# Kernel optimization log

Measured on AMD Instinct MI355X. Metric: run time of the kernel, lower is better.

The kernel has to match this reference:

```python
import jax, jax.numpy as jnp
from jax import lax
import numpy as np

VOCAB, EMB, HID, NCLS = 50257, 768, 512, 5
B, T = 32, 1024


def setup_inputs() -> dict:
    key = jax.random.key(0)
    ks = jax.random.split(key, 12)
    s_e = 1.0  # torch nn.Embedding default init is N(0,1)
    def unif(k, shape, fan):
        bound = 1.0 / np.sqrt(fan)
        return jax.random.uniform(k, shape, jnp.float32, -bound, bound)
    return {
        "x": jax.random.randint(ks[0], (B, T), 0, VOCAB),
        "emb": jax.random.normal(ks[1], (VOCAB, EMB), jnp.float32) * s_e,
        "w_ih0": unif(ks[2], (4 * HID, EMB), HID),
        "w_hh0": unif(ks[3], (4 * HID, HID), HID),
        "b_ih0": unif(ks[4], (4 * HID,), HID),
        "b_hh0": unif(ks[5], (4 * HID,), HID),
        "w_ih1": unif(ks[6], (4 * HID, HID), HID),
        "w_hh1": unif(ks[7], (4 * HID, HID), HID),
        "b_ih1": unif(ks[8], (4 * HID,), HID),
        "b_hh1": unif(ks[9], (4 * HID,), HID),
        "fc_w": unif(ks[10], (NCLS, HID), HID),
        "fc_b": unif(ks[11], (NCLS,), HID),
    }


def _lstm_layer(x, w_ih, w_hh, b_ih, b_hh):
    # x: [B, T, D] -> hs: [B, T, H]; PyTorch gate order: i, f, g, o
    Bb = x.shape[0]
    H = w_hh.shape[1]
    gx = jnp.einsum('btd,gd->btg', x, w_ih) + b_ih + b_hh  # [B, T, 4H]
    gx_t = jnp.swapaxes(gx, 0, 1)  # [T, B, 4H]
    h0 = jnp.zeros((Bb, H), x.dtype)
    c0 = jnp.zeros((Bb, H), x.dtype)

    def step(carry, g_in):
        h, c = carry
        g = g_in + h @ w_hh.T
        i, f, gg, o = jnp.split(g, 4, axis=-1)
        c = jax.nn.sigmoid(f) * c + jax.nn.sigmoid(i) * jnp.tanh(gg)
        h = jax.nn.sigmoid(o) * jnp.tanh(c)
        return (h, c), h

    _, hs = lax.scan(step, (h0, c0), gx_t)
    return jnp.swapaxes(hs, 0, 1)  # [B, T, H]


def reference(x, emb, w_ih0, w_hh0, b_ih0, b_hh0, w_ih1, w_hh1, b_ih1, b_hh1, fc_w, fc_b):
    e = emb[x]                                   # [B, T, EMB]
    h1 = _lstm_layer(e, w_ih0, w_hh0, b_ih0, b_hh0)   # [B, T, H]
    # inter-layer dropout and final dropout are identity in eval mode
    h2 = _lstm_layer(h1, w_ih1, w_hh1, b_ih1, b_hh1)  # [B, T, H]
    last = h2[:, -1, :]                          # [B, H]
    return last @ fc_w.T + fc_b                  # [B, NCLS]
```

## Files before the change

### kernel.cpp

```cpp
#include <hip/hip_runtime.h>
#include <stdint.h>

typedef _Float16 f16;
typedef _Float16 half8 __attribute__((ext_vector_type(8)));
typedef float f32x4 __attribute__((ext_vector_type(4)));
typedef unsigned long long u64;

#define T_SEQ 1024
#define NWG 136
#define FS 32

#define WS_FLAGS_BYTES (NWG * 128)
#define WS_H0 32768
#define WS_H1 (WS_H0 + 131072)
#define WS_E  (WS_H1 + 65536)
#define ESLOT 24576
#define HPLANE 16384

static __device__ __forceinline__ half8 ld_h8(const f16* p) {
    u64 lo = __hip_atomic_load((const u64*)p,     __ATOMIC_RELAXED, __HIP_MEMORY_SCOPE_AGENT);
    u64 hi = __hip_atomic_load((const u64*)p + 1, __ATOMIC_RELAXED, __HIP_MEMORY_SCOPE_AGENT);
    union { u64 q[2]; half8 v; } u; u.q[0] = lo; u.q[1] = hi; return u.v;
}

static __device__ __forceinline__ void poll64(uint32_t* flags, int base, int n,
                                              uint32_t need, int lane) {
    int idx = (base + (lane < n ? lane : 0)) * FS;
    while (true) {
        uint32_t v = __hip_atomic_load(flags + idx, __ATOMIC_RELAXED,
                                       __HIP_MEMORY_SCOPE_AGENT);
        if (__all(v >= need)) break;
        __builtin_amdgcn_s_sleep(1);
    }
    __builtin_amdgcn_sched_barrier(0);
}

static __device__ __forceinline__ void poll2(uint32_t* flags, uint32_t needA,
                                             uint32_t needB, int lane) {
    while (true) {
        uint32_t a = __hip_atomic_load(flags + lane * FS, __ATOMIC_RELAXED,
                                       __HIP_MEMORY_SCOPE_AGENT);
        uint32_t b = __hip_atomic_load(flags + (64 + lane) * FS, __ATOMIC_RELAXED,
                                       __HIP_MEMORY_SCOPE_AGENT);
        if (__all((a >= needA) && (b >= needB))) break;
        __builtin_amdgcn_s_sleep(1);
    }
    __builtin_amdgcn_sched_barrier(0);
}

__global__ void __launch_bounds__(256, 1)
lstm_fused(const int* __restrict__ x, const float* __restrict__ emb,
           const float* __restrict__ w_ih0, const float* __restrict__ w_hh0,
           const float* __restrict__ b_ih0, const float* __restrict__ b_hh0,
           const float* __restrict__ w_ih1, const float* __restrict__ w_hh1,
           const float* __restrict__ b_ih1, const float* __restrict__ b_hh1,
           const float* __restrict__ fc_w, const float* __restrict__ fc_b,
           float* __restrict__ out, uint8_t* __restrict__ ws)
{
    const int wg   = blockIdx.x;
    const int tid  = threadIdx.x;
    const int lane = tid & 63;
    const int wave = tid >> 6;
    const int mtile = wave >> 1;
    const int ntile = wave & 1;
    const int r8   = lane & 15;
    const int kgb  = lane >> 4;

    uint32_t* flags = (uint32_t*)ws;
    f16* h0buf = (f16*)(ws + WS_H0);
    f16* h1buf = (f16*)(ws + WS_H1);
    f16* ering = (f16*)(ws + WS_E);

    if (wg >= 128) {
        const int p = wg - 128;
        auto gather = [&](int t) {
#pragma unroll
            for (int rr = 0; rr < 2; ++rr) {
                int idx = rr * 256 + tid;
                if (idx < 384) {
                    int bl = idx / 96, seg = idx % 96, k0 = seg * 8;
                    int b = p * 4 + bl;
                    int tok = x[b * T_SEQ + t];
                    const float* src = emb + (size_t)tok * 768 + k0;
                    float4 v0 = ((const float4*)src)[0];
                    float4 v1 = ((const float4*)src)[1];
                    union { half8 h; u64 q[2]; } u;
                    u.h[0] = (f16)v0.x; u.h[1] = (f16)v0.y; u.h[2] = (f16)v0.z; u.h[3] = (f16)v0.w;
                    u.h[4] = (f16)v1.x; u.h[5] = (f16)v1.y; u.h[6] = (f16)v1.z; u.h[7] = (f16)v1.w;
                    u64* dst = (u64*)(ering + (size_t)(t & 3) * ESLOT + ((size_t)seg * 32 + b) * 8);
                    __hip_atomic_store(dst,     u.q[0], __ATOMIC_RELAXED, __HIP_MEMORY_SCOPE_AGENT);
                    __hip_atomic_store(dst + 1, u.q[1], __ATOMIC_RELAXED, __HIP_MEMORY_SCOPE_AGENT);
                }
            }
        };
        gather(0); gather(1); gather(2);
        asm volatile("s_waitcnt vmcnt(0)" ::: "memory");
        __syncthreads();
        if (tid == 0)
            __hip_atomic_store(flags + wg * FS, 3u, __ATOMIC_RELAXED, __HIP_MEMORY_SCOPE_AGENT);
        for (int s = 0;; ++s) {
            int g = s + 3;
            if (g >= T_SEQ) {
                if (tid == 0)
                    __hip_atomic_store(flags + wg * FS, (uint32_t)(T_SEQ + 8),
                                       __ATOMIC_RELAXED, __HIP_MEMORY_SCOPE_AGENT);
                break;
            }
            poll64(flags, 0, 64, (uint32_t)(s + 1), lane);
            gather(g);
            asm volatile("s_waitcnt vmcnt(0)" ::: "memory");
            __syncthreads();
            if (tid == 0)
                __hip_atomic_store(flags + wg * FS, (uint32_t)(s + 4),
                                   __ATOMIC_RELAXED, __HIP_MEMORY_SCOPE_AGENT);
        }
        return;
    }

    const bool isL0 = (wg < 64);
    const int wloc  = isL0 ? wg : wg - 64;
    const int j0    = wloc * 8;

    __shared__ float accs[32][33];
    __shared__ float bias_lds[32];
    __shared__ f16   hsh[32][8];
    __shared__ f16   stage[16384];

    const int nrow = ((ntile * 2 + (r8 >> 3)) << 9) + j0 + (r8 & 7);
    half8 breg[40];
    if (isL0) {
#pragma unroll
        for (int kc = 0; kc < 40; ++kc) {
            int k = kc * 32 + kgb * 8;
            const float* src = (k < 768) ? (w_ih0 + (size_t)nrow * 768 + k)
                                         : (w_hh0 + (size_t)nrow * 512 + (k - 768));
            half8 v;
#pragma unroll
            for (int e = 0; e < 8; ++e) v[e] = (f16)src[e];
            breg[kc] = v;
        }
    } else {
#pragma unroll
        for (int kc = 0; kc < 32; ++kc) {
            int k = kc * 32 + kgb * 8;
            const float* src = (k < 512) ? (w_ih1 + (size_t)nrow * 512 + k)
                                         : (w_hh1 + (size_t)nrow * 512 + (k - 512));
            half8 v;
#pragma unroll
            for (int e = 0; e < 8; ++e) v[e] = (f16)src[e];
            breg[kc] = v;
        }
    }
    if (tid < 32) {
        int n2 = ((tid >> 3) << 9) + j0 + (tid & 7);
        bias_lds[tid] = isL0 ? (b_ih0[n2] + b_hh0[n2]) : (b_ih1[n2] + b_hh1[n2]);
    }

    {
        int gid = wg * 256 + tid;
        if (gid < 8192) {
            u64* base = (gid < 4096) ? (u64*)(h0buf + 3 * HPLANE)
                                     : (u64*)(h1buf + 1 * HPLANE);
            __hip_atomic_store(base + (gid & 4095), 0ULL,
                               __ATOMIC_RELAXED, __HIP_MEMORY_SCOPE_AGENT);
        }
    }
    asm volatile("s_waitcnt vmcnt(0)" ::: "memory");
    __syncthreads();
    if (tid == 0)
        __hip_atomic_store(flags + wg * FS, isL0 ? 1u : 2u,
                           __ATOMIC_RELAXED, __HIP_MEMORY_SCOPE_AGENT);

    float cst = 0.f;
    const int tb = tid >> 3, tj = tid & 7;
    const int arow = mtile * 16 + r8;

    const int sBeg = isL0 ? 0 : 1;
    const int sEnd = isL0 ? T_SEQ : T_SEQ + 1;

    for (int s = sBeg; s < sEnd; ++s) {
        f32x4 acc0 = {0.f, 0.f, 0.f, 0.f}, acc1 = {0.f, 0.f, 0.f, 0.f};
        if (isL0) {
            poll64(flags, 128, 8, (uint32_t)(s + 1), lane);
            const f16* pe = ering + (size_t)(s & 3) * ESLOT;
            half8 ea[24];
#pragma unroll
            for (int kc = 0; kc < 24; ++kc)
                ea[kc] = ld_h8(pe + (((size_t)(kc * 4 + kgb) * 32 + arow) << 3));
            poll2(flags, (uint32_t)(s + 1), (uint32_t)(s > 0 ? s - 1 : 0), lane);
            const f16* ph = h0buf + (size_t)((s + 3) & 3) * HPLANE;
#pragma unroll
            for (int kc = 0; kc < 24; ++kc) {
                if (kc & 1) acc1 = __builtin_amdgcn_mfma_f32_16x16x32_f16(ea[kc], breg[kc], acc1, 0, 0, 0);
                else        acc0 = __builtin_amdgcn_mfma_f32_16x16x32_f16(ea[kc], breg[kc], acc0, 0, 0, 0);
            }
#pragma unroll
            for (int kc = 24; kc < 40; ++kc) {
                half8 a = ld_h8(ph + ((((size_t)(kc - 24) * 4 + kgb) * 32 + arow) << 3));
                if (kc & 1) acc1 = __builtin_amdgcn_mfma_f32_16x16x32_f16(a, breg[kc], acc1, 0, 0, 0);
                else        acc0 = __builtin_amdgcn_mfma_f32_16x16x32_f16(a, breg[kc], acc0, 0, 0, 0);
            }
        } else {
            poll64(flags, 0, 64, (uint32_t)(s + 1), lane);
            const f16* pa = h0buf + (size_t)((s + 3) & 3) * HPLANE;
            half8 av[16];
#pragma unroll
            for (int kc = 0; kc < 16; ++kc)
                av[kc] = ld_h8(pa + (((size_t)(kc * 4 + kgb) * 32 + arow) << 3));
            poll64(flags, 64, 64, (uint32_t)(s + 1), lane);
            const f16* pb = h1buf + (size_t)(s & 1) * HPLANE;
#pragma unroll
            for (int kc = 0; kc < 16; ++kc) {
                if (kc & 1) acc1 = __builtin_amdgcn_mfma_f32_16x16x32_f16(av[kc], breg[kc], acc1, 0, 0, 0);
                else        acc0 = __builtin_amdgcn_mfma_f32_16x16x32_f16(av[kc], breg[kc], acc0, 0, 0, 0);
            }
#pragma unroll
            for (int kc = 16; kc < 32; ++kc) {
                half8 a = ld_h8(pb + ((((size_t)(kc - 16) * 4 + kgb) * 32 + arow) << 3));
                if (kc & 1) acc1 = __builtin_amdgcn_mfma_f32_16x16x32_f16(a, breg[kc], acc1, 0, 0, 0);
                else        acc0 = __builtin_amdgcn_mfma_f32_16x16x32_f16(a, breg[kc], acc0, 0, 0, 0);
            }
        }
        {
            f32x4 accv = acc0 + acc1;
            const int crow0 = mtile * 16 + (lane >> 4) * 4;
            const int ccol  = ntile * 16 + r8;
#pragma unroll
            for (int q = 0; q < 4; ++q) accs[crow0 + q][ccol] = accv[q];
        }
        __syncthreads();
        {
            float gi = accs[tb][tj]      + bias_lds[tj];
            float gf = accs[tb][8 + tj]  + bias_lds[8 + tj];
            float gg = accs[tb][16 + tj] + bias_lds[16 + tj];
            float go = accs[tb][24 + tj] + bias_lds[24 + tj];
            float si = __builtin_amdgcn_rcpf(1.f + __expf(-gi));
            float sf = __builtin_amdgcn_rcpf(1.f + __expf(-gf));
            float so = __builtin_amdgcn_rcpf(1.f + __expf(-go));
            float tg = 1.f - 2.f * __builtin_amdgcn_rcpf(__expf(2.f * gg) + 1.f);
            cst = sf * cst + si * tg;
            float hv = so * (1.f - 2.f * __builtin_amdgcn_rcpf(__expf(2.f * cst) + 1.f));
            hsh[tb][tj] = (f16)hv;
        }
        __syncthreads();
        if (tid < 32) {
            f16* plane = isL0 ? (h0buf + (size_t)(s & 3) * HPLANE)
                              : (h1buf + (size_t)((s + 1) & 1) * HPLANE);
            u64* dst = (u64*)plane + ((size_t)wloc * 32 + tid) * 2;
            const u64* srcp = (const u64*)hsh + tid * 2;
            u64 q0 = srcp[0], q1 = srcp[1];
            __hip_atomic_store(dst,     q0, __ATOMIC_RELAXED, __HIP_MEMORY_SCOPE_AGENT);
            __hip_atomic_store(dst + 1, q1, __ATOMIC_RELAXED, __HIP_MEMORY_SCOPE_AGENT);
        }
        if (tid == 0) {
            asm volatile("s_waitcnt vmcnt(0)" ::: "memory");
            __hip_atomic_store(flags + wg * FS, (uint32_t)(s + 2),
                               __ATOMIC_RELAXED, __HIP_MEMORY_SCOPE_AGENT);
        }
    }

    if (wg == 0) {
        poll64(flags, 64, 64, (uint32_t)(T_SEQ + 2), lane);
        u64* h2g = (u64*)(h1buf + 1 * HPLANE);
        u64* stg = (u64*)stage;
        for (int i = tid; i < 4096; i += 256)
            stg[i] = __hip_atomic_load(h2g + i, __ATOMIC_RELAXED, __HIP_MEMORY_SCOPE_AGENT);
        __syncthreads();
        if (tid < 160) {
            int b = tid / 5, n = tid % 5;
            const f16* h2 = stage;
            float fsum = fc_b[n];
#pragma unroll 8
            for (int j = 0; j < 512; ++j)
                fsum += (float)h2[((j >> 3) * 32 + b) * 8 + (j & 7)] * fc_w[n * 512 + j];
            out[b * 5 + n] = fsum;
        }
    }
}

extern "C" void kernel_launch(void* const* d_in, const int* in_sizes, int n_in,
                              void* d_out, int out_size, void* d_ws, size_t ws_size,
                              hipStream_t stream) {
    (void)in_sizes; (void)n_in; (void)out_size; (void)ws_size;
    hipMemsetAsync(d_ws, 0, WS_FLAGS_BYTES, stream);
    lstm_fused<<<dim3(NWG), dim3(256), 0, stream>>>(
        (const int*)d_in[0],  (const float*)d_in[1],
        (const float*)d_in[2], (const float*)d_in[3],
        (const float*)d_in[4], (const float*)d_in[5],
        (const float*)d_in[6], (const float*)d_in[7],
        (const float*)d_in[8], (const float*)d_in[9],
        (const float*)d_in[10], (const float*)d_in[11],
        (float*)d_out, (uint8_t*)d_ws);
}
```

Baseline: 4.309 ms.

## Stage LSTM weights in LDS, poll flags with one wave, pack flag slots

Recurrent and input weights now live in 80KB of shared memory instead of 160 VGPRs per lane. They are loaded once by two waves and read from LDS at every MFMA step. Flag polling is done by wave 0 only, followed by a workgroup barrier. The flag stride shrinks from 32 to 8 words, so polls touch fewer cache lines. All A-operand loads for the hidden state are issued before the MFMA chains to hide load latency. In exchange, every timestep pays for LDS weight reads and extra barriers on a recurrence that is bound by latency.

```diff
diff --git a/kernel.cpp b/kernel.cpp
--- a/kernel.cpp
+++ b/kernel.cpp
@@ -8,9 +8,9 @@
 
 #define T_SEQ 1024
 #define NWG 136
-#define FS 32
-
-#define WS_FLAGS_BYTES (NWG * 128)
+#define FS 8
+
+#define WS_FLAGS_BYTES 8192
 #define WS_H0 32768
 #define WS_H1 (WS_H0 + 131072)
 #define WS_E  (WS_H1 + 65536)
@@ -106,7 +106,8 @@
                                        __ATOMIC_RELAXED, __HIP_MEMORY_SCOPE_AGENT);
                 break;
             }
-            poll64(flags, 0, 64, (uint32_t)(s + 1), lane);
+            if (wave == 0) poll64(flags, 0, 64, (uint32_t)(s + 1), lane);
+            __syncthreads();
             gather(g);
             asm volatile("s_waitcnt vmcnt(0)" ::: "memory");
             __syncthreads();
@@ -121,34 +122,35 @@
     const int wloc  = isL0 ? wg : wg - 64;
     const int j0    = wloc * 8;
 
+    __shared__ half8 wlds[2 * 40 * 64];
     __shared__ float accs[32][33];
     __shared__ float bias_lds[32];
     __shared__ f16   hsh[32][8];
-    __shared__ f16   stage[16384];
 
     const int nrow = ((ntile * 2 + (r8 >> 3)) << 9) + j0 + (r8 & 7);
-    half8 breg[40];
-    if (isL0) {
-#pragma unroll
-        for (int kc = 0; kc < 40; ++kc) {
-            int k = kc * 32 + kgb * 8;
-            const float* src = (k < 768) ? (w_ih0 + (size_t)nrow * 768 + k)
-                                         : (w_hh0 + (size_t)nrow * 512 + (k - 768));
-            half8 v;
-#pragma unroll
-            for (int e = 0; e < 8; ++e) v[e] = (f16)src[e];
-            breg[kc] = v;
-        }
-    } else {
-#pragma unroll
-        for (int kc = 0; kc < 32; ++kc) {
-            int k = kc * 32 + kgb * 8;
-            const float* src = (k < 512) ? (w_ih1 + (size_t)nrow * 512 + k)
-                                         : (w_hh1 + (size_t)nrow * 512 + (k - 512));
-            half8 v;
-#pragma unroll
-            for (int e = 0; e < 8; ++e) v[e] = (f16)src[e];
-            breg[kc] = v;
+    if (wave < 2) {
+        if (isL0) {
+#pragma unroll
+            for (int kc = 0; kc < 40; ++kc) {
+                int k = kc * 32 + kgb * 8;
+                const float* src = (k < 768) ? (w_ih0 + (size_t)nrow * 768 + k)
+                                             : (w_hh0 + (size_t)nrow * 512 + (k - 768));
+                half8 v;
+#pragma unroll
+                for (int e = 0; e < 8; ++e) v[e] = (f16)src[e];
+                wlds[ntile * 2560 + kc * 64 + lane] = v;
+            }
+        } else {
+#pragma unroll
+            for (int kc = 0; kc < 32; ++kc) {
+                int k = kc * 32 + kgb * 8;
+                const float* src = (k < 512) ? (w_ih1 + (size_t)nrow * 512 + k)
+                                             : (w_hh1 + (size_t)nrow * 512 + (k - 512));
+                half8 v;
+#pragma unroll
+                for (int e = 0; e < 8; ++e) v[e] = (f16)src[e];
+                wlds[ntile * 2560 + kc * 64 + lane] = v;
+            }
         }
     }
     if (tid < 32) {
@@ -174,6 +176,7 @@
     float cst = 0.f;
     const int tb = tid >> 3, tj = tid & 7;
     const int arow = mtile * 16 + r8;
+    const half8* wbase = wlds + ntile * 2560;
 
     const int sBeg = isL0 ? 0 : 1;
     const int sEnd = isL0 ? T_SEQ : T_SEQ + 1;
@@ -181,44 +184,58 @@
     for (int s = sBeg; s < sEnd; ++s) {
         f32x4 acc0 = {0.f, 0.f, 0.f, 0.f}, acc1 = {0.f, 0.f, 0.f, 0.f};
         if (isL0) {
-            poll64(flags, 128, 8, (uint32_t)(s + 1), lane);
+            if (wave == 0) poll64(flags, 128, 8, (uint32_t)(s + 1), lane);
+            __syncthreads();
             const f16* pe = ering + (size_t)(s & 3) * ESLOT;
             half8 ea[24];
 #pragma unroll
             for (int kc = 0; kc < 24; ++kc)
                 ea[kc] = ld_h8(pe + (((size_t)(kc * 4 + kgb) * 32 + arow) << 3));
-            poll2(flags, (uint32_t)(s + 1), (uint32_t)(s > 0 ? s - 1 : 0), lane);
+            if (wave == 0) poll2(flags, (uint32_t)(s + 1), (uint32_t)(s > 0 ? s - 1 : 0), lane);
+            __syncthreads();
             const f16* ph = h0buf + (size_t)((s + 3) & 3) * HPLANE;
+            half8 av[16];
+#pragma unroll
+            for (int kc = 0; kc < 16; ++kc)
+                av[kc] = ld_h8(ph + (((size_t)(kc * 4 + kgb) * 32 + arow) << 3));
 #pragma unroll
             for (int kc = 0; kc < 24; ++kc) {
-                if (kc & 1) acc1 = __builtin_amdgcn_mfma_f32_16x16x32_f16(ea[kc], breg[kc], acc1, 0, 0, 0);
-                else        acc0 = __builtin_amdgcn_mfma_f32_16x16x32_f16(ea[kc], breg[kc], acc0, 0, 0, 0);
-            }
-#pragma unroll
-            for (int kc = 24; kc < 40; ++kc) {
-                half8 a = ld_h8(ph + ((((size_t)(kc - 24) * 4 + kgb) * 32 + arow) << 3));
-                if (kc & 1) acc1 = __builtin_amdgcn_mfma_f32_16x16x32_f16(a, breg[kc], acc1, 0, 0, 0);
-                else        acc0 = __builtin_amdgcn_mfma_f32_16x16x32_f16(a, breg[kc], acc0, 0, 0, 0);
+                half8 bw = wbase[kc * 64 + lane];
+                if (kc & 1) acc1 = __builtin_amdgcn_mfma_f32_16x16x32_f16(ea[kc], bw, acc1, 0, 0, 0);
+                else        acc0 = __builtin_amdgcn_mfma_f32_16x16x32_f16(ea[kc], bw, acc0, 0, 0, 0);
+            }
+#pragma unroll
+            for (int kc = 0; kc < 16; ++kc) {
+                half8 bw = wbase[(24 + kc) * 64 + lane];
+                if (kc & 1) acc1 = __builtin_amdgcn_mfma_f32_16x16x32_f16(av[kc], bw, acc1, 0, 0, 0);
+                else        acc0 = __builtin_amdgcn_mfma_f32_16x16x32_f16(av[kc], bw, acc0, 0, 0, 0);
             }
         } else {
-            poll64(flags, 0, 64, (uint32_t)(s + 1), lane);
+            if (wave == 0) poll64(flags, 0, 64, (uint32_t)(s + 1), lane);
+            __syncthreads();
             const f16* pa = h0buf + (size_t)((s + 3) & 3) * HPLANE;
             half8 av[16];
 #pragma unroll
             for (int kc = 0; kc < 16; ++kc)
                 av[kc] = ld_h8(pa + (((size_t)(kc * 4 + kgb) * 32 + arow) << 3));
-            poll64(flags, 64, 64, (uint32_t)(s + 1), lane);
+            if (wave == 0) poll64(flags, 64, 64, (uint32_t)(s + 1), lane);
+            __syncthreads();
             const f16* pb = h1buf + (size_t)(s & 1) * HPLANE;
+            half8 bv[16];
+#pragma unroll
+            for (int kc = 0; kc < 16; ++kc)
+                bv[kc] = ld_h8(pb + (((size_t)(kc * 4 + kgb) * 32 + arow) << 3));
 #pragma unroll
             for (int kc = 0; kc < 16; ++kc) {
-                if (kc & 1) acc1 = __builtin_amdgcn_mfma_f32_16x16x32_f16(av[kc], breg[kc], acc1, 0, 0, 0);
-                else        acc0 = __builtin_amdgcn_mfma_f32_16x16x32_f16(av[kc], breg[kc], acc0, 0, 0, 0);
-            }
-#pragma unroll
-            for (int kc = 16; kc < 32; ++kc) {
-                half8 a = ld_h8(pb + ((((size_t)(kc - 16) * 4 + kgb) * 32 + arow) << 3));
-                if (kc & 1) acc1 = __builtin_amdgcn_mfma_f32_16x16x32_f16(a, breg[kc], acc1, 0, 0, 0);
-                else        acc0 = __builtin_amdgcn_mfma_f32_16x16x32_f16(a, breg[kc], acc0, 0, 0, 0);
+                half8 bw = wbase[kc * 64 + lane];
+                if (kc & 1) acc1 = __builtin_amdgcn_mfma_f32_16x16x32_f16(av[kc], bw, acc1, 0, 0, 0);
+                else        acc0 = __builtin_amdgcn_mfma_f32_16x16x32_f16(av[kc], bw, acc0, 0, 0, 0);
+            }
+#pragma unroll
+            for (int kc = 0; kc < 16; ++kc) {
+                half8 bw = wbase[(16 + kc) * 64 + lane];
+                if (kc & 1) acc1 = __builtin_amdgcn_mfma_f32_16x16x32_f16(bv[kc], bw, acc1, 0, 0, 0);
+                else        acc0 = __builtin_amdgcn_mfma_f32_16x16x32_f16(bv[kc], bw, acc0, 0, 0, 0);
             }
         }
         {
@@ -260,15 +277,16 @@
     }
 
     if (wg == 0) {
-        poll64(flags, 64, 64, (uint32_t)(T_SEQ + 2), lane);
+        if (wave == 0) poll64(flags, 64, 64, (uint32_t)(T_SEQ + 2), lane);
+        __syncthreads();
         u64* h2g = (u64*)(h1buf + 1 * HPLANE);
-        u64* stg = (u64*)stage;
+        u64* stg = (u64*)wlds;
         for (int i = tid; i < 4096; i += 256)
             stg[i] = __hip_atomic_load(h2g + i, __ATOMIC_RELAXED, __HIP_MEMORY_SCOPE_AGENT);
         __syncthreads();
         if (tid < 160) {
             int b = tid / 5, n = tid % 5;
-            const f16* h2 = stage;
+            const f16* h2 = (const f16*)stg;
             float fsum = fc_b[n];
 #pragma unroll 8
             for (int j = 0; j < 512; ++j)
```

Result: slower. 4.781 ms (+10.9%).

## Replace per-workgroup flag polling with slotted atomic counters and deeper h1 ring

Applied to the files above, without the earlier changes.

Replaces the per-workgroup flag array, which consumers polled across 64 lanes, with per-timestep slot counters: 8 counters per ring slot, each incremented by a group of 8 producer workgroups, so a wait reads only 16 words. The h1 buffer becomes a 4-deep ring, which loosens the coupling between layers, and L0 now loads its h operands up front before the MFMAs. Embedding producers signal through per-slot counters. The intent is less polling traffic and latency on the per-step critical path. In exchange it adds atomic fetch_add contention and relies on counter wraparound across 8 slots being correct, and several vmcnt waits were dropped before signaling, which risks memory-ordering bugs.

```diff
diff --git a/kernel.cpp b/kernel.cpp
--- a/kernel.cpp
+++ b/kernel.cpp
@@ -8,14 +8,18 @@
 
 #define T_SEQ 1024
 #define NWG 136
-#define FS 32
-
-#define WS_FLAGS_BYTES (NWG * 128)
-#define WS_H0 32768
+
+#define R0L(slot) ((uint32_t*)(ws + ((((slot) & 7)) * 128)))
+#define R1L(slot) ((uint32_t*)(ws + 1024 + ((((slot) & 7)) * 128)))
+#define WS_H0 4096
 #define WS_H1 (WS_H0 + 131072)
-#define WS_E  (WS_H1 + 65536)
+#define WS_E  (WS_H1 + 131072)
 #define ESLOT 24576
 #define HPLANE 16384
+
+static __device__ __forceinline__ uint32_t needOf(int it) {
+    return it < 0 ? 0u : 8u * (((uint32_t)it >> 3) + 1u);
+}
 
 static __device__ __forceinline__ half8 ld_h8(const f16* p) {
     u64 lo = __hip_atomic_load((const u64*)p,     __ATOMIC_RELAXED, __HIP_MEMORY_SCOPE_AGENT);
@@ -23,26 +27,21 @@
     union { u64 q[2]; half8 v; } u; u.q[0] = lo; u.q[1] = hi; return u.v;
 }
 
-static __device__ __forceinline__ void poll64(uint32_t* flags, int base, int n,
-                                              uint32_t need, int lane) {
-    int idx = (base + (lane < n ? lane : 0)) * FS;
+static __device__ __forceinline__ void poll1(uint32_t* w, uint32_t need) {
+    while (__hip_atomic_load(w, __ATOMIC_RELAXED, __HIP_MEMORY_SCOPE_AGENT) < need)
+        __builtin_amdgcn_s_sleep(1);
+    __builtin_amdgcn_sched_barrier(0);
+}
+
+static __device__ __forceinline__ void poll16(uint32_t* a, uint32_t na,
+                                              uint32_t* b, uint32_t nb, int lane) {
+    uint32_t* addr; uint32_t need;
+    if (lane < 8)       { addr = a + lane;       need = na; }
+    else if (lane < 16) { addr = b + (lane - 8); need = nb; }
+    else                { addr = a;              need = 0;  }
     while (true) {
-        uint32_t v = __hip_atomic_load(flags + idx, __ATOMIC_RELAXED,
-                                       __HIP_MEMORY_SCOPE_AGENT);
+        uint32_t v = __hip_atomic_load(addr, __ATOMIC_RELAXED, __HIP_MEMORY_SCOPE_AGENT);
         if (__all(v >= need)) break;
-        __builtin_amdgcn_s_sleep(1);
-    }
-    __builtin_amdgcn_sched_barrier(0);
-}
-
-static __device__ __forceinline__ void poll2(uint32_t* flags, uint32_t needA,
-                                             uint32_t needB, int lane) {
-    while (true) {
-        uint32_t a = __hip_atomic_load(flags + lane * FS, __ATOMIC_RELAXED,
-                                       __HIP_MEMORY_SCOPE_AGENT);
-        uint32_t b = __hip_atomic_load(flags + (64 + lane) * FS, __ATOMIC_RELAXED,
-                                       __HIP_MEMORY_SCOPE_AGENT);
-        if (__all((a >= needA) && (b >= needB))) break;
         __builtin_amdgcn_s_sleep(1);
     }
     __builtin_amdgcn_sched_barrier(0);
@@ -66,7 +65,8 @@
     const int r8   = lane & 15;
     const int kgb  = lane >> 4;
 
-    uint32_t* flags = (uint32_t*)ws;
+    uint32_t* EW = (uint32_t*)(ws + 2048);
+    uint32_t* IW = (uint32_t*)(ws + 2176);
     f16* h0buf = (f16*)(ws + WS_H0);
     f16* h1buf = (f16*)(ws + WS_H1);
     f16* ering = (f16*)(ws + WS_E);
@@ -94,25 +94,20 @@
             }
         };
         gather(0); gather(1); gather(2);
-        asm volatile("s_waitcnt vmcnt(0)" ::: "memory");
         __syncthreads();
-        if (tid == 0)
-            __hip_atomic_store(flags + wg * FS, 3u, __ATOMIC_RELAXED, __HIP_MEMORY_SCOPE_AGENT);
-        for (int s = 0;; ++s) {
-            int g = s + 3;
-            if (g >= T_SEQ) {
-                if (tid == 0)
-                    __hip_atomic_store(flags + wg * FS, (uint32_t)(T_SEQ + 8),
-                                       __ATOMIC_RELAXED, __HIP_MEMORY_SCOPE_AGENT);
-                break;
-            }
-            poll64(flags, 0, 64, (uint32_t)(s + 1), lane);
+        if (tid == 0) {
+            __hip_atomic_fetch_add(EW + 0, 1u, __ATOMIC_RELAXED, __HIP_MEMORY_SCOPE_AGENT);
+            __hip_atomic_fetch_add(EW + 1, 1u, __ATOMIC_RELAXED, __HIP_MEMORY_SCOPE_AGENT);
+            __hip_atomic_fetch_add(EW + 2, 1u, __ATOMIC_RELAXED, __HIP_MEMORY_SCOPE_AGENT);
+        }
+        for (int g = 3; g < T_SEQ; ++g) {
+            if (g >= 4)
+                poll16(R0L(g - 4), needOf(g - 4), R0L(g - 4), 0u, lane);
             gather(g);
-            asm volatile("s_waitcnt vmcnt(0)" ::: "memory");
             __syncthreads();
             if (tid == 0)
-                __hip_atomic_store(flags + wg * FS, (uint32_t)(s + 4),
-                                   __ATOMIC_RELAXED, __HIP_MEMORY_SCOPE_AGENT);
+                __hip_atomic_fetch_add(EW + (g & 3), 1u,
+                                       __ATOMIC_RELAXED, __HIP_MEMORY_SCOPE_AGENT);
         }
         return;
     }
@@ -160,108 +155,113 @@
         int gid = wg * 256 + tid;
         if (gid < 8192) {
             u64* base = (gid < 4096) ? (u64*)(h0buf + 3 * HPLANE)
-                                     : (u64*)(h1buf + 1 * HPLANE);
+                                     : (u64*)(h1buf + 3 * HPLANE);
             __hip_atomic_store(base + (gid & 4095), 0ULL,
                                __ATOMIC_RELAXED, __HIP_MEMORY_SCOPE_AGENT);
         }
     }
-    asm volatile("s_waitcnt vmcnt(0)" ::: "memory");
     __syncthreads();
-    if (tid == 0)
-        __hip_atomic_store(flags + wg * FS, isL0 ? 1u : 2u,
-                           __ATOMIC_RELAXED, __HIP_MEMORY_SCOPE_AGENT);
+    if (wg < 32 && tid == 0)
+        __hip_atomic_fetch_add(IW, 1u, __ATOMIC_RELAXED, __HIP_MEMORY_SCOPE_AGENT);
+    poll1(IW, 32u);
 
     float cst = 0.f;
     const int tb = tid >> 3, tj = tid & 7;
     const int arow = mtile * 16 + r8;
 
-    const int sBeg = isL0 ? 0 : 1;
     const int sEnd = isL0 ? T_SEQ : T_SEQ + 1;
 
-    for (int s = sBeg; s < sEnd; ++s) {
-        f32x4 acc0 = {0.f, 0.f, 0.f, 0.f}, acc1 = {0.f, 0.f, 0.f, 0.f};
-        if (isL0) {
-            poll64(flags, 128, 8, (uint32_t)(s + 1), lane);
-            const f16* pe = ering + (size_t)(s & 3) * ESLOT;
-            half8 ea[24];
-#pragma unroll
-            for (int kc = 0; kc < 24; ++kc)
-                ea[kc] = ld_h8(pe + (((size_t)(kc * 4 + kgb) * 32 + arow) << 3));
-            poll2(flags, (uint32_t)(s + 1), (uint32_t)(s > 0 ? s - 1 : 0), lane);
-            const f16* ph = h0buf + (size_t)((s + 3) & 3) * HPLANE;
-#pragma unroll
-            for (int kc = 0; kc < 24; ++kc) {
-                if (kc & 1) acc1 = __builtin_amdgcn_mfma_f32_16x16x32_f16(ea[kc], breg[kc], acc1, 0, 0, 0);
-                else        acc0 = __builtin_amdgcn_mfma_f32_16x16x32_f16(ea[kc], breg[kc], acc0, 0, 0, 0);
-            }
-#pragma unroll
-            for (int kc = 24; kc < 40; ++kc) {
-                half8 a = ld_h8(ph + ((((size_t)(kc - 24) * 4 + kgb) * 32 + arow) << 3));
-                if (kc & 1) acc1 = __builtin_amdgcn_mfma_f32_16x16x32_f16(a, breg[kc], acc1, 0, 0, 0);
-                else        acc0 = __builtin_amdgcn_mfma_f32_16x16x32_f16(a, breg[kc], acc0, 0, 0, 0);
-            }
-        } else {
-            poll64(flags, 0, 64, (uint32_t)(s + 1), lane);
-            const f16* pa = h0buf + (size_t)((s + 3) & 3) * HPLANE;
-            half8 av[16];
-#pragma unroll
-            for (int kc = 0; kc < 16; ++kc)
-                av[kc] = ld_h8(pa + (((size_t)(kc * 4 + kgb) * 32 + arow) << 3));
-            poll64(flags, 64, 64, (uint32_t)(s + 1), lane);
-            const f16* pb = h1buf + (size_t)(s & 1) * HPLANE;
-#pragma unroll
-            for (int kc = 0; kc < 16; ++kc) {
-                if (kc & 1) acc1 = __builtin_amdgcn_mfma_f32_16x16x32_f16(av[kc], breg[kc], acc1, 0, 0, 0);
-                else        acc0 = __builtin_amdgcn_mfma_f32_16x16x32_f16(av[kc], breg[kc], acc0, 0, 0, 0);
-            }
-#pragma unroll
-            for (int kc = 16; kc < 32; ++kc) {
-                half8 a = ld_h8(pb + ((((size_t)(kc - 16) * 4 + kgb) * 32 + arow) << 3));
-                if (kc & 1) acc1 = __builtin_amdgcn_mfma_f32_16x16x32_f16(a, breg[kc], acc1, 0, 0, 0);
-                else        acc0 = __builtin_amdgcn_mfma_f32_16x16x32_f16(a, breg[kc], acc0, 0, 0, 0);
-            }
-        }
-        {
-            f32x4 accv = acc0 + acc1;
-            const int crow0 = mtile * 16 + (lane >> 4) * 4;
-            const int ccol  = ntile * 16 + r8;
-#pragma unroll
-            for (int q = 0; q < 4; ++q) accs[crow0 + q][ccol] = accv[q];
-        }
-        __syncthreads();
-        {
-            float gi = accs[tb][tj]      + bias_lds[tj];
-            float gf = accs[tb][8 + tj]  + bias_lds[8 + tj];
-            float gg = accs[tb][16 + tj] + bias_lds[16 + tj];
-            float go = accs[tb][24 + tj] + bias_lds[24 + tj];
-            float si = __builtin_amdgcn_rcpf(1.f + __expf(-gi));
-            float sf = __builtin_amdgcn_rcpf(1.f + __expf(-gf));
-            float so = __builtin_amdgcn_rcpf(1.f + __expf(-go));
-            float tg = 1.f - 2.f * __builtin_amdgcn_rcpf(__expf(2.f * gg) + 1.f);
-            cst = sf * cst + si * tg;
-            float hv = so * (1.f - 2.f * __builtin_amdgcn_rcpf(__expf(2.f * cst) + 1.f));
-            hsh[tb][tj] = (f16)hv;
-        }
-        __syncthreads();
-        if (tid < 32) {
-            f16* plane = isL0 ? (h0buf + (size_t)(s & 3) * HPLANE)
-                              : (h1buf + (size_t)((s + 1) & 1) * HPLANE);
-            u64* dst = (u64*)plane + ((size_t)wloc * 32 + tid) * 2;
-            const u64* srcp = (const u64*)hsh + tid * 2;
-            u64 q0 = srcp[0], q1 = srcp[1];
-            __hip_atomic_store(dst,     q0, __ATOMIC_RELAXED, __HIP_MEMORY_SCOPE_AGENT);
-            __hip_atomic_store(dst + 1, q1, __ATOMIC_RELAXED, __HIP_MEMORY_SCOPE_AGENT);
+    for (int s = 0; s < sEnd; ++s) {
+        const bool active = isL0 || (s >= 1);
+        if (active) {
+            f32x4 acc0 = {0.f, 0.f, 0.f, 0.f}, acc1 = {0.f, 0.f, 0.f, 0.f};
+            if (isL0) {
+                poll1(EW + (s & 3), 8u * (((uint32_t)s >> 2) + 1u));
+                const f16* pe = ering + (size_t)(s & 3) * ESLOT;
+                half8 ea[24];
+#pragma unroll
+                for (int kc = 0; kc < 24; ++kc)
+                    ea[kc] = ld_h8(pe + (((size_t)(kc * 4 + kgb) * 32 + arow) << 3));
+                poll16(R0L(s - 1), needOf(s - 1), R1L(s - 3), needOf(s - 3), lane);
+                const f16* ph = h0buf + (size_t)((s + 3) & 3) * HPLANE;
+                half8 av[16];
+#pragma unroll
+                for (int kc = 0; kc < 16; ++kc)
+                    av[kc] = ld_h8(ph + (((size_t)(kc * 4 + kgb) * 32 + arow) << 3));
+#pragma unroll
+                for (int kc = 0; kc < 24; ++kc) {
+                    if (kc & 1) acc1 = __builtin_amdgcn_mfma_f32_16x16x32_f16(ea[kc], breg[kc], acc1, 0, 0, 0);
+                    else        acc0 = __builtin_amdgcn_mfma_f32_16x16x32_f16(ea[kc], breg[kc], acc0, 0, 0, 0);
+                }
+#pragma unroll
+                for (int kc = 0; kc < 16; ++kc) {
+                    if (kc & 1) acc1 = __builtin_amdgcn_mfma_f32_16x16x32_f16(av[kc], breg[24 + kc], acc1, 0, 0, 0);
+                    else        acc0 = __builtin_amdgcn_mfma_f32_16x16x32_f16(av[kc], breg[24 + kc], acc0, 0, 0, 0);
+                }
+            } else {
+                poll16(R0L(s - 1), needOf(s - 1), R1L(s - 1), needOf(s - 1), lane);
+                const f16* pa = h0buf + (size_t)((s + 3) & 3) * HPLANE;
+                const f16* pb = h1buf + (size_t)((s + 2) & 3) * HPLANE;
+                half8 av[16], bv[16];
+#pragma unroll
+                for (int kc = 0; kc < 16; ++kc)
+                    av[kc] = ld_h8(pa + (((size_t)(kc * 4 + kgb) * 32 + arow) << 3));
+#pragma unroll
+                for (int kc = 0; kc < 16; ++kc)
+                    bv[kc] = ld_h8(pb + (((size_t)(kc * 4 + kgb) * 32 + arow) << 3));
+#pragma unroll
+                for (int kc = 0; kc < 16; ++kc) {
+                    if (kc & 1) acc1 = __builtin_amdgcn_mfma_f32_16x16x32_f16(av[kc], breg[kc], acc1, 0, 0, 0);
+                    else        acc0 = __builtin_amdgcn_mfma_f32_16x16x32_f16(av[kc], breg[kc], acc0, 0, 0, 0);
+                }
+#pragma unroll
+                for (int kc = 0; kc < 16; ++kc) {
+                    if (kc & 1) acc1 = __builtin_amdgcn_mfma_f32_16x16x32_f16(bv[kc], breg[16 + kc], acc1, 0, 0, 0);
+                    else        acc0 = __builtin_amdgcn_mfma_f32_16x16x32_f16(bv[kc], breg[16 + kc], acc0, 0, 0, 0);
+                }
+            }
+            {
+                f32x4 accv = acc0 + acc1;
+                const int crow0 = mtile * 16 + (lane >> 4) * 4;
+                const int ccol  = ntile * 16 + r8;
+#pragma unroll
+                for (int q = 0; q < 4; ++q) accs[crow0 + q][ccol] = accv[q];
+            }
+            __syncthreads();
+            {
+                float gi = accs[tb][tj]      + bias_lds[tj];
+                float gf = accs[tb][8 + tj]  + bias_lds[8 + tj];
+                float gg = accs[tb][16 + tj] + bias_lds[16 + tj];
+                float go = accs[tb][24 + tj] + bias_lds[24 + tj];
+                float si = __builtin_amdgcn_rcpf(1.f + __expf(-gi));
+                float sf = __builtin_amdgcn_rcpf(1.f + __expf(-gf));
+                float so = __builtin_amdgcn_rcpf(1.f + __expf(-go));
+                float tg = 1.f - 2.f * __builtin_amdgcn_rcpf(__expf(2.f * gg) + 1.f);
+                cst = sf * cst + si * tg;
+                float hv = so * (1.f - 2.f * __builtin_amdgcn_rcpf(__expf(2.f * cst) + 1.f));
+                hsh[tb][tj] = (f16)hv;
+            }
+            __syncthreads();
+            if (tid < 32) {
+                f16* plane = isL0 ? (h0buf + (size_t)(s & 3) * HPLANE)
+                                  : (h1buf + (size_t)((s + 3) & 3) * HPLANE);
+                u64* dst = (u64*)plane + ((size_t)wloc * 32 + tid) * 2;
+                const u64* srcp = (const u64*)hsh + tid * 2;
+                u64 q0 = srcp[0], q1 = srcp[1];
+                __hip_atomic_store(dst,     q0, __ATOMIC_RELAXED, __HIP_MEMORY_SCOPE_AGENT);
+                __hip_atomic_store(dst + 1, q1, __ATOMIC_RELAXED, __HIP_MEMORY_SCOPE_AGENT);
+            }
         }
         if (tid == 0) {
             asm volatile("s_waitcnt vmcnt(0)" ::: "memory");
-            __hip_atomic_store(flags + wg * FS, (uint32_t)(s + 2),
-                               __ATOMIC_RELAXED, __HIP_MEMORY_SCOPE_AGENT);
+            uint32_t* ctr = (isL0 ? R0L(s) : R1L(s)) + (wloc >> 3);
+            __hip_atomic_fetch_add(ctr, 1u, __ATOMIC_RELAXED, __HIP_MEMORY_SCOPE_AGENT);
         }
     }
 
     if (wg == 0) {
-        poll64(flags, 64, 64, (uint32_t)(T_SEQ + 2), lane);
-        u64* h2g = (u64*)(h1buf + 1 * HPLANE);
+        poll16(R1L(0), needOf(T_SEQ), R1L(0), needOf(T_SEQ), lane);
+        u64* h2g = (u64*)(h1buf + 3 * HPLANE);
         u64* stg = (u64*)stage;
         for (int i = tid; i < 4096; i += 256)
             stg[i] = __hip_atomic_load(h2g + i, __ATOMIC_RELAXED, __HIP_MEMORY_SCOPE_AGENT);
@@ -282,7 +282,7 @@
                               void* d_out, int out_size, void* d_ws, size_t ws_size,
                               hipStream_t stream) {
     (void)in_sizes; (void)n_in; (void)out_size; (void)ws_size;
-    hipMemsetAsync(d_ws, 0, WS_FLAGS_BYTES, stream);
+    hipMemsetAsync(d_ws, 0, 4096, stream);
     lstm_fused<<<dim3(NWG), dim3(256), 0, stream>>>(
         (const int*)d_in[0],  (const float*)d_in[1],
         (const float*)d_in[2], (const float*)d_in[3],
```

Result: slower. 5.227 ms (+21.3%).

## Split flag arrays, use single combined poll, and stage A operands cooperatively in LDS

Applied to the files above, without the earlier changes.

Flags move into separate compact arrays for layer-0, layer-1 and the producer workgroups, packed at 32-byte stride instead of 128. Each step now waits on all dependencies in one combined poll. Every wave then loads a disjoint slice of the shared A operand (embeddings and hidden states) from global memory into LDS, so waves sharing an M tile no longer load the same data twice. The embedding ring shrinks to 3 slots and the producers key off layer-0 progress directly. This cuts redundant global loads per step, but adds an LDS round trip and a barrier, and removes the overlap between embedding loads and the hidden-state wait.

```diff
diff --git a/kernel.cpp b/kernel.cpp
--- a/kernel.cpp
+++ b/kernel.cpp
@@ -8,41 +8,60 @@
 
 #define T_SEQ 1024
 #define NWG 136
-#define FS 32
-
-#define WS_FLAGS_BYTES (NWG * 128)
-#define WS_H0 32768
+#define FS 8
+#define DE 3
+#define HPLANE 16384
+#define ESLOT 24576
+
+#define OFF_FA 0
+#define OFF_FB 2048
+#define OFF_FP 4096
+#define WS_H0 8192
 #define WS_H1 (WS_H0 + 131072)
 #define WS_E  (WS_H1 + 65536)
-#define ESLOT 24576
-#define HPLANE 16384
-
+
+static __device__ __forceinline__ u64 ld64(const u64* p) {
+    return __hip_atomic_load(p, __ATOMIC_RELAXED, __HIP_MEMORY_SCOPE_AGENT);
+}
+static __device__ __forceinline__ void st64(u64* p, u64 v) {
+    __hip_atomic_store(p, v, __ATOMIC_RELAXED, __HIP_MEMORY_SCOPE_AGENT);
+}
+static __device__ __forceinline__ uint32_t ld32(const uint32_t* p) {
+    return __hip_atomic_load(p, __ATOMIC_RELAXED, __HIP_MEMORY_SCOPE_AGENT);
+}
+static __device__ __forceinline__ void st32(uint32_t* p, uint32_t v) {
+    __hip_atomic_store(p, v, __ATOMIC_RELAXED, __HIP_MEMORY_SCOPE_AGENT);
+}
+static __device__ __forceinline__ half8 h8(u64 lo, u64 hi) {
+    union { u64 q[2]; half8 v; } u; u.q[0] = lo; u.q[1] = hi; return u.v;
+}
 static __device__ __forceinline__ half8 ld_h8(const f16* p) {
-    u64 lo = __hip_atomic_load((const u64*)p,     __ATOMIC_RELAXED, __HIP_MEMORY_SCOPE_AGENT);
-    u64 hi = __hip_atomic_load((const u64*)p + 1, __ATOMIC_RELAXED, __HIP_MEMORY_SCOPE_AGENT);
-    union { u64 q[2]; half8 v; } u; u.q[0] = lo; u.q[1] = hi; return u.v;
-}
-
-static __device__ __forceinline__ void poll64(uint32_t* flags, int base, int n,
-                                              uint32_t need, int lane) {
-    int idx = (base + (lane < n ? lane : 0)) * FS;
+    u64 lo = ld64((const u64*)p);
+    u64 hi = ld64((const u64*)p + 1);
+    return h8(lo, hi);
+}
+static __device__ __forceinline__ void pollM(const uint32_t* fA, uint32_t needA,
+                                             const uint32_t* fB, uint32_t needB,
+                                             const uint32_t* fP, uint32_t needP,
+                                             int lane) {
+    const uint32_t* pa = fA + (size_t)lane * FS;
+    const uint32_t* pb = fB + (size_t)lane * FS;
+    const uint32_t* pp = fP + (size_t)(lane & 7) * FS;
     while (true) {
-        uint32_t v = __hip_atomic_load(flags + idx, __ATOMIC_RELAXED,
-                                       __HIP_MEMORY_SCOPE_AGENT);
+        uint32_t va = ld32(pa);
+        uint32_t vb = ld32(pb);
+        uint32_t vp = ld32(pp);
+        if (__all((va >= needA) && (vb >= needB) && (vp >= needP))) break;
+        __builtin_amdgcn_s_sleep(1);
+    }
+    __builtin_amdgcn_sched_barrier(0);
+}
+static __device__ __forceinline__ void pollA(const uint32_t* flags, int n,
+                                             uint32_t need, int lane) {
+    const uint32_t* p = flags + (size_t)(lane < n ? lane : 0) * FS;
+    while (true) {
+        uint32_t v = ld32(p);
         if (__all(v >= need)) break;
-        __builtin_amdgcn_s_sleep(1);
-    }
-    __builtin_amdgcn_sched_barrier(0);
-}
-
-static __device__ __forceinline__ void poll2(uint32_t* flags, uint32_t needA,
-                                             uint32_t needB, int lane) {
-    while (true) {
-        uint32_t a = __hip_atomic_load(flags + lane * FS, __ATOMIC_RELAXED,
-                                       __HIP_MEMORY_SCOPE_AGENT);
-        uint32_t b = __hip_atomic_load(flags + (64 + lane) * FS, __ATOMIC_RELAXED,
-                                       __HIP_MEMORY_SCOPE_AGENT);
-        if (__all((a >= needA) && (b >= needB))) break;
         __builtin_amdgcn_s_sleep(1);
     }
     __builtin_amdgcn_sched_barrier(0);
@@ -65,20 +84,23 @@
     const int ntile = wave & 1;
     const int r8   = lane & 15;
     const int kgb  = lane >> 4;
-
-    uint32_t* flags = (uint32_t*)ws;
+    const int tb = tid >> 3, tj = tid & 7;
+
+    uint32_t* fA = (uint32_t*)(ws + OFF_FA);
+    uint32_t* fB = (uint32_t*)(ws + OFF_FB);
+    uint32_t* fP = (uint32_t*)(ws + OFF_FP);
     f16* h0buf = (f16*)(ws + WS_H0);
     f16* h1buf = (f16*)(ws + WS_H1);
     f16* ering = (f16*)(ws + WS_E);
 
     if (wg >= 128) {
         const int p = wg - 128;
-        auto gather = [&](int t) {
+        auto gather = [&](int t, int slot) {
 #pragma unroll
             for (int rr = 0; rr < 2; ++rr) {
-                int idx = rr * 256 + tid;
-                if (idx < 384) {
-                    int bl = idx / 96, seg = idx % 96, k0 = seg * 8;
+                int idx2 = rr * 256 + tid;
+                if (idx2 < 384) {
+                    int bl = idx2 / 96, seg = idx2 % 96, k0 = seg * 8;
                     int b = p * 4 + bl;
                     int tok = x[b * T_SEQ + t];
                     const float* src = emb + (size_t)tok * 768 + k0;
@@ -87,32 +109,21 @@
                     union { half8 h; u64 q[2]; } u;
                     u.h[0] = (f16)v0.x; u.h[1] = (f16)v0.y; u.h[2] = (f16)v0.z; u.h[3] = (f16)v0.w;
                     u.h[4] = (f16)v1.x; u.h[5] = (f16)v1.y; u.h[6] = (f16)v1.z; u.h[7] = (f16)v1.w;
-                    u64* dst = (u64*)(ering + (size_t)(t & 3) * ESLOT + ((size_t)seg * 32 + b) * 8);
-                    __hip_atomic_store(dst,     u.q[0], __ATOMIC_RELAXED, __HIP_MEMORY_SCOPE_AGENT);
-                    __hip_atomic_store(dst + 1, u.q[1], __ATOMIC_RELAXED, __HIP_MEMORY_SCOPE_AGENT);
+                    u64* dst = (u64*)(ering + (size_t)slot * ESLOT + ((size_t)seg * 32 + b) * 8);
+                    st64(dst, u.q[0]); st64(dst + 1, u.q[1]);
                 }
             }
         };
-        gather(0); gather(1); gather(2);
+        gather(0, 0); gather(1, 1); gather(2, 2);
         asm volatile("s_waitcnt vmcnt(0)" ::: "memory");
         __syncthreads();
-        if (tid == 0)
-            __hip_atomic_store(flags + wg * FS, 3u, __ATOMIC_RELAXED, __HIP_MEMORY_SCOPE_AGENT);
-        for (int s = 0;; ++s) {
-            int g = s + 3;
-            if (g >= T_SEQ) {
-                if (tid == 0)
-                    __hip_atomic_store(flags + wg * FS, (uint32_t)(T_SEQ + 8),
-                                       __ATOMIC_RELAXED, __HIP_MEMORY_SCOPE_AGENT);
-                break;
-            }
-            poll64(flags, 0, 64, (uint32_t)(s + 1), lane);
-            gather(g);
+        if (tid == 0) st32(fP + p * FS, 3u);
+        for (int g = 3; g < T_SEQ; ++g) {
+            pollA(fA, 64, (uint32_t)(g - 1), lane);
+            gather(g, g % DE);
             asm volatile("s_waitcnt vmcnt(0)" ::: "memory");
             __syncthreads();
-            if (tid == 0)
-                __hip_atomic_store(flags + wg * FS, (uint32_t)(s + 4),
-                                   __ATOMIC_RELAXED, __HIP_MEMORY_SCOPE_AGENT);
+            if (tid == 0) st32(fP + p * FS, (uint32_t)(g + 1));
         }
         return;
     }
@@ -121,10 +132,10 @@
     const int wloc  = isL0 ? wg : wg - 64;
     const int j0    = wloc * 8;
 
+    __shared__ half8 astage[80 * 64];
     __shared__ float accs[32][33];
     __shared__ float bias_lds[32];
     __shared__ f16   hsh[32][8];
-    __shared__ f16   stage[16384];
 
     const int nrow = ((ntile * 2 + (r8 >> 3)) << 9) + j0 + (r8 & 7);
     half8 breg[40];
@@ -161,70 +172,59 @@
         if (gid < 8192) {
             u64* base = (gid < 4096) ? (u64*)(h0buf + 3 * HPLANE)
                                      : (u64*)(h1buf + 1 * HPLANE);
-            __hip_atomic_store(base + (gid & 4095), 0ULL,
-                               __ATOMIC_RELAXED, __HIP_MEMORY_SCOPE_AGENT);
+            st64(base + (gid & 4095), 0ULL);
         }
     }
     asm volatile("s_waitcnt vmcnt(0)" ::: "memory");
     __syncthreads();
-    if (tid == 0)
-        __hip_atomic_store(flags + wg * FS, isL0 ? 1u : 2u,
-                           __ATOMIC_RELAXED, __HIP_MEMORY_SCOPE_AGENT);
+    if (tid == 0) st32((isL0 ? fA : fB) + wloc * FS, isL0 ? 1u : 2u);
 
     float cst = 0.f;
-    const int tb = tid >> 3, tj = tid & 7;
-    const int arow = mtile * 16 + r8;
+    const int crow0 = mtile * 16 + (lane >> 4) * 4;
+    const int ccol  = ntile * 16 + r8;
 
     const int sBeg = isL0 ? 0 : 1;
     const int sEnd = isL0 ? T_SEQ : T_SEQ + 1;
+    const int NKC  = isL0 ? 40 : 32;
+    const int NST  = isL0 ? 20 : 16;
 
     for (int s = sBeg; s < sEnd; ++s) {
+        if (isL0) pollM(fA, (uint32_t)(s + 1), fB, (uint32_t)(s > 0 ? s - 1 : 0),
+                        fP, (uint32_t)(s + 1), lane);
+        else      pollM(fA, (uint32_t)(s + 1), fB, (uint32_t)(s + 1),
+                        fP, 0u, lane);
+        const f16* pe = ering + (size_t)(s % DE) * ESLOT;
+        const f16* ph0 = h0buf + (size_t)((s + 3) & 3) * HPLANE;
+        const f16* ph1 = h1buf + (size_t)(s & 1) * HPLANE;
+        {
+            half8 stg[20];
+#pragma unroll
+            for (int j = 0; j < 20; ++j) {
+                if (j >= NST) break;
+                int f = wave * NST + j;
+                int mt = f / NKC, kc = f % NKC;
+                const f16* base; int kk;
+                if (isL0) { base = (kc < 24) ? pe : ph0; kk = (kc < 24) ? kc : kc - 24; }
+                else      { base = (kc < 16) ? ph0 : ph1; kk = (kc < 16) ? kc : kc - 16; }
+                stg[j] = ld_h8(base + (((size_t)(kk * 4 + kgb) * 32 + mt * 16 + r8) << 3));
+            }
+#pragma unroll
+            for (int j = 0; j < 20; ++j) {
+                if (j >= NST) break;
+                astage[(size_t)(wave * NST + j) * 64 + lane] = stg[j];
+            }
+        }
+        __syncthreads();
         f32x4 acc0 = {0.f, 0.f, 0.f, 0.f}, acc1 = {0.f, 0.f, 0.f, 0.f};
-        if (isL0) {
-            poll64(flags, 128, 8, (uint32_t)(s + 1), lane);
-            const f16* pe = ering + (size_t)(s & 3) * ESLOT;
-            half8 ea[24];
-#pragma unroll
-            for (int kc = 0; kc < 24; ++kc)
-                ea[kc] = ld_h8(pe + (((size_t)(kc * 4 + kgb) * 32 + arow) << 3));
-            poll2(flags, (uint32_t)(s + 1), (uint32_t)(s > 0 ? s - 1 : 0), lane);
-            const f16* ph = h0buf + (size_t)((s + 3) & 3) * HPLANE;
-#pragma unroll
-            for (int kc = 0; kc < 24; ++kc) {
-                if (kc & 1) acc1 = __builtin_amdgcn_mfma_f32_16x16x32_f16(ea[kc], breg[kc], acc1, 0, 0, 0);
-                else        acc0 = __builtin_amdgcn_mfma_f32_16x16x32_f16(ea[kc], breg[kc], acc0, 0, 0, 0);
-            }
-#pragma unroll
-            for (int kc = 24; kc < 40; ++kc) {
-                half8 a = ld_h8(ph + ((((size_t)(kc - 24) * 4 + kgb) * 32 + arow) << 3));
-                if (kc & 1) acc1 = __builtin_amdgcn_mfma_f32_16x16x32_f16(a, breg[kc], acc1, 0, 0, 0);
-                else        acc0 = __builtin_amdgcn_mfma_f32_16x16x32_f16(a, breg[kc], acc0, 0, 0, 0);
-            }
-        } else {
-            poll64(flags, 0, 64, (uint32_t)(s + 1), lane);
-            const f16* pa = h0buf + (size_t)((s + 3) & 3) * HPLANE;
-            half8 av[16];
-#pragma unroll
-            for (int kc = 0; kc < 16; ++kc)
-                av[kc] = ld_h8(pa + (((size_t)(kc * 4 + kgb) * 32 + arow) << 3));
-            poll64(flags, 64, 64, (uint32_t)(s + 1), lane);
-            const f16* pb = h1buf + (size_t)(s & 1) * HPLANE;
-#pragma unroll
-            for (int kc = 0; kc < 16; ++kc) {
-                if (kc & 1) acc1 = __builtin_amdgcn_mfma_f32_16x16x32_f16(av[kc], breg[kc], acc1, 0, 0, 0);
-                else        acc0 = __builtin_amdgcn_mfma_f32_16x16x32_f16(av[kc], breg[kc], acc0, 0, 0, 0);
-            }
-#pragma unroll
-            for (int kc = 16; kc < 32; ++kc) {
-                half8 a = ld_h8(pb + ((((size_t)(kc - 16) * 4 + kgb) * 32 + arow) << 3));
-                if (kc & 1) acc1 = __builtin_amdgcn_mfma_f32_16x16x32_f16(a, breg[kc], acc1, 0, 0, 0);
-                else        acc0 = __builtin_amdgcn_mfma_f32_16x16x32_f16(a, breg[kc], acc0, 0, 0, 0);
-            }
+#pragma unroll
+        for (int kc = 0; kc < 40; ++kc) {
+            if (kc >= NKC) break;
+            half8 a = astage[(size_t)(mtile * NKC + kc) * 64 + lane];
+            if (kc & 1) acc1 = __builtin_amdgcn_mfma_f32_16x16x32_f16(a, breg[kc], acc1, 0, 0, 0);
+            else        acc0 = __builtin_amdgcn_mfma_f32_16x16x32_f16(a, breg[kc], acc0, 0, 0, 0);
         }
         {
             f32x4 accv = acc0 + acc1;
-            const int crow0 = mtile * 16 + (lane >> 4) * 4;
-            const int ccol  = ntile * 16 + r8;
 #pragma unroll
             for (int q = 0; q < 4; ++q) accs[crow0 + q][ccol] = accv[q];
         }
@@ -249,26 +249,24 @@
             u64* dst = (u64*)plane + ((size_t)wloc * 32 + tid) * 2;
             const u64* srcp = (const u64*)hsh + tid * 2;
             u64 q0 = srcp[0], q1 = srcp[1];
-            __hip_atomic_store(dst,     q0, __ATOMIC_RELAXED, __HIP_MEMORY_SCOPE_AGENT);
-            __hip_atomic_store(dst + 1, q1, __ATOMIC_RELAXED, __HIP_MEMORY_SCOPE_AGENT);
+            st64(dst, q0); st64(dst + 1, q1);
         }
         if (tid == 0) {
             asm volatile("s_waitcnt vmcnt(0)" ::: "memory");
-            __hip_atomic_store(flags + wg * FS, (uint32_t)(s + 2),
-                               __ATOMIC_RELAXED, __HIP_MEMORY_SCOPE_AGENT);
+            st32((isL0 ? fA : fB) + wloc * FS, (uint32_t)(s + 2));
         }
     }
 
     if (wg == 0) {
-        poll64(flags, 64, 64, (uint32_t)(T_SEQ + 2), lane);
-        u64* h2g = (u64*)(h1buf + 1 * HPLANE);
-        u64* stg = (u64*)stage;
+        pollA(fB, 64, (uint32_t)(T_SEQ + 2), lane);
+        const u64* h2g = (const u64*)(h1buf + 1 * HPLANE);
+        u64* stg = (u64*)astage;
         for (int i = tid; i < 4096; i += 256)
-            stg[i] = __hip_atomic_load(h2g + i, __ATOMIC_RELAXED, __HIP_MEMORY_SCOPE_AGENT);
+            stg[i] = ld64(h2g + i);
         __syncthreads();
         if (tid < 160) {
             int b = tid / 5, n = tid % 5;
-            const f16* h2 = stage;
+            const f16* h2 = (const f16*)stg;
             float fsum = fc_b[n];
 #pragma unroll 8
             for (int j = 0; j < 512; ++j)
@@ -282,7 +280,7 @@
                               void* d_out, int out_size, void* d_ws, size_t ws_size,
                               hipStream_t stream) {
     (void)in_sizes; (void)n_in; (void)out_size; (void)ws_size;
-    hipMemsetAsync(d_ws, 0, WS_FLAGS_BYTES, stream);
+    hipMemsetAsync(d_ws, 0, 8192, stream);
     lstm_fused<<<dim3(NWG), dim3(256), 0, stream>>>(
         (const int*)d_in[0],  (const float*)d_in[1],
         (const float*)d_in[2], (const float*)d_in[3],
```

New measurement: 16.77 ms. +289.1%, slower.
